# Kernel optimization log

Hardware: AMD Instinct MI355X
Metric: run time of the kernel (lower is better)

## Reference

```python
import jax, jax.numpy as jnp
import numpy as np

N_NODES = 100000
N_EDGES = 1600000
D_FEAT = 128
EPS = 0.0

def setup_inputs() -> dict:
    key = jax.random.key(0)
    k1, k2, k3 = jax.random.split(key, 3)
    feat = jax.random.normal(k1, (N_NODES, D_FEAT), dtype=jnp.float32)
    src = jax.random.randint(k2, (N_EDGES,), 0, N_NODES, dtype=jnp.int32)
    dst = jax.random.randint(k3, (N_EDGES,), 0, N_NODES, dtype=jnp.int32)
    return {"feat": feat, "src": src, "dst": dst}

def reference(feat, src, dst):
    # copy_u: gather messages from edge sources; sum-reduce into destinations
    msgs = feat[src]                                   # [E, D]
    neigh = jax.ops.segment_sum(msgs, dst, num_segments=N_NODES)  # [N, D]
    # (1 + eps) * feat_dst + aggregated neighbors
    return (1.0 + EPS) * feat + neigh
```

## Files before the change

kernel.cpp:

```cpp
#include <hip/hip_runtime.h>

#define D_FEAT 128
#define CAP 64
typedef unsigned int uint32;


__global__ void k_zero(uint32* __restrict__ p, int n) {
    int stride = gridDim.x * blockDim.x;
    for (int i = blockIdx.x * blockDim.x + threadIdx.x; i < n; i += stride)
        p[i] = 0u;
}

__global__ void k_fill_slack4(const int* __restrict__ src, const int* __restrict__ dst,
                              uint32* __restrict__ cur, int* __restrict__ adj, int e) {
    int i = blockIdx.x * blockDim.x + threadIdx.x;
    int nvec = e >> 2;
    if (i < nvec) {
        int4 s4 = ((const int4*)src)[i];
        int4 d4 = ((const int4*)dst)[i];
        uint32 p0 = atomicAdd(&cur[d4.x], 1u);
        uint32 p1 = atomicAdd(&cur[d4.y], 1u);
        uint32 p2 = atomicAdd(&cur[d4.z], 1u);
        uint32 p3 = atomicAdd(&cur[d4.w], 1u);
        if (p0 < CAP) adj[(size_t)d4.x * CAP + p0] = s4.x;
        if (p1 < CAP) adj[(size_t)d4.y * CAP + p1] = s4.y;
        if (p2 < CAP) adj[(size_t)d4.z * CAP + p2] = s4.z;
        if (p3 < CAP) adj[(size_t)d4.w * CAP + p3] = s4.w;
    }
    if (i == 0) {
        for (int k = nvec << 2; k < e; ++k) {
            int d = dst[k];
            uint32 p = atomicAdd(&cur[d], 1u);
            if (p < CAP) adj[(size_t)d * CAP + p] = src[k];
        }
    }
}

__global__ void k_gather4(const float4* __restrict__ feat4,
                          const uint32* __restrict__ deg,
                          const int* __restrict__ adj,
                          float4* __restrict__ out4, int n_nodes) {
    int gtid = blockIdx.x * blockDim.x + threadIdx.x;
    int wave = gtid >> 6;
    int lane = gtid & 63;
    int half = lane >> 5;
    int l    = lane & 31;
    int node = wave * 2 + half;
    if (node >= n_nodes) return;
    float4 acc = feat4[(size_t)node * 32 + l];
    int cnt = min((int)deg[node], CAP);
    for (int b = 0; b < cnt; b += 32) {
        int m = min(32, cnt - b);
        int a = (l < m) ? adj[(size_t)node * CAP + b + l] : 0;
        for (int j = 0; j < m; ++j) {
            int s = __shfl(a, j, 32);
            float4 v = feat4[(size_t)s * 32 + l];
            acc.x += v.x; acc.y += v.y; acc.z += v.z; acc.w += v.w;
        }
    }
    out4[(size_t)node * 32 + l] = acc;
}


__global__ void k_hist(const int* __restrict__ dst, uint32* __restrict__ deg, int e) {
    int i = blockIdx.x * blockDim.x + threadIdx.x;
    if (i < e) atomicAdd(&deg[dst[i]], 1u);
}

__global__ void k_scan1(const uint32* __restrict__ deg, uint32* __restrict__ offs,
                        uint32* __restrict__ bsum, int n) {
    __shared__ uint32 lds[256];
    int t = threadIdx.x;
    int i0 = blockIdx.x * 1024 + t * 4;
    uint32 v[4];
    for (int k = 0; k < 4; ++k) { int i = i0 + k; v[k] = (i < n) ? deg[i] : 0u; }
    uint32 tsum = v[0] + v[1] + v[2] + v[3];
    lds[t] = tsum; __syncthreads();
    uint32 run = tsum;
    for (int off = 1; off < 256; off <<= 1) {
        uint32 add = (t >= off) ? lds[t - off] : 0u; __syncthreads();
        run += add; lds[t] = run; __syncthreads();
    }
    uint32 p = run - tsum;
    for (int k = 0; k < 4; ++k) { int i = i0 + k; if (i < n) offs[i] = p; p += v[k]; }
    if (t == 255) bsum[blockIdx.x] = run;
}

__global__ void k_scan2(uint32* __restrict__ bsum, int nb) {
    __shared__ uint32 lds[256];
    int t = threadIdx.x;
    uint32 v = (t < nb) ? bsum[t] : 0u;
    lds[t] = v; __syncthreads();
    uint32 run = v;
    for (int off = 1; off < 256; off <<= 1) {
        uint32 add = (t >= off) ? lds[t - off] : 0u; __syncthreads();
        run += add; lds[t] = run; __syncthreads();
    }
    if (t < nb) bsum[t] = run - v;
}

__global__ void k_scan3(uint32* __restrict__ offs, uint32* __restrict__ cur,
                        const uint32* __restrict__ bsum, int n) {
    int i0 = blockIdx.x * 1024 + threadIdx.x * 4;
    uint32 add = bsum[blockIdx.x];
    for (int k = 0; k < 4; ++k) {
        int i = i0 + k;
        if (i < n) { uint32 o = offs[i] + add; offs[i] = o; cur[i] = o; }
    }
}

__global__ void k_fill(const int* __restrict__ src, const int* __restrict__ dst,
                       uint32* __restrict__ cur, int* __restrict__ adj, int e) {
    int i = blockIdx.x * blockDim.x + threadIdx.x;
    if (i < e) {
        int d = dst[i];
        uint32 p = atomicAdd(&cur[d], 1u);
        adj[p] = src[i];
    }
}

__global__ void k_gather(const float2* __restrict__ feat2,
                         const uint32* __restrict__ offs,
                         const uint32* __restrict__ endp,
                         const int* __restrict__ adj,
                         float2* __restrict__ out2, int n_nodes) {
    int gtid = blockIdx.x * blockDim.x + threadIdx.x;
    int node = gtid >> 6;
    int lane = gtid & 63;
    if (node >= n_nodes) return;
    float2 acc = feat2[(size_t)node * 64 + lane];
    int e0 = (int)offs[node];
    int e1 = (int)endp[node];
    for (int b = e0; b < e1; b += 64) {
        int cnt = min(64, e1 - b);
        int a = (lane < cnt) ? adj[b + lane] : 0;
        for (int j = 0; j < cnt; ++j) {
            int s = __shfl(a, j);
            float2 v = feat2[(size_t)s * 64 + lane];
            acc.x += v.x; acc.y += v.y;
        }
    }
    out2[(size_t)node * 64 + lane] = acc;
}


__global__ void init_out_kernel(const float4* __restrict__ feat,
                                float4* __restrict__ out, int n4) {
    int stride = gridDim.x * blockDim.x;
    for (int i = blockIdx.x * blockDim.x + threadIdx.x; i < n4; i += stride)
        out[i] = feat[i];
}

__global__ void scatter_edges_kernel(const float* __restrict__ feat,
                                     const int* __restrict__ src,
                                     const int* __restrict__ dst,
                                     float* __restrict__ out, int n_edges) {
    long long stride = (long long)gridDim.x * blockDim.x;
    long long total  = (long long)n_edges * 32;
    for (long long gtid = (long long)blockIdx.x * blockDim.x + threadIdx.x;
         gtid < total; gtid += stride) {
        int edge = (int)(gtid >> 5);
        int lane = (int)(gtid & 31);
        int s = src[edge];
        int d = dst[edge];
        const float4 v =
            *reinterpret_cast<const float4*>(feat + (size_t)s * D_FEAT + lane * 4);
        float* op = out + (size_t)d * D_FEAT + lane * 4;
        unsafeAtomicAdd(op + 0, v.x);
        unsafeAtomicAdd(op + 1, v.y);
        unsafeAtomicAdd(op + 2, v.z);
        unsafeAtomicAdd(op + 3, v.w);
    }
}

extern "C" void kernel_launch(void* const* d_in, const int* in_sizes, int n_in,
                              void* d_out, int out_size, void* d_ws, size_t ws_size,
                              hipStream_t stream) {
    const float* feat = (const float*)d_in[0];
    const int*   src  = (const int*)d_in[1];
    const int*   dst  = (const int*)d_in[2];
    float*       out  = (float*)d_out;

    int n_feat  = in_sizes[0];
    int n_edges = in_sizes[1];
    int n_nodes = n_feat / D_FEAT;
    int blk = 256;

    size_t need0 = ((size_t)n_nodes * CAP + n_nodes) * sizeof(uint32);
    if (ws_size >= need0) {
        int*    adj = (int*)d_ws;
        uint32* cur = (uint32*)(adj + (size_t)n_nodes * CAP);

        k_zero<<<256, blk, 0, stream>>>(cur, n_nodes);
        int nvec = n_edges >> 2;
        k_fill_slack4<<<(nvec + blk - 1) / blk, blk, 0, stream>>>(
            src, dst, cur, adj, n_edges);

        int nwaves = (n_nodes + 1) / 2;
        long long gthreads = (long long)nwaves * 64;
        k_gather4<<<(int)((gthreads + blk - 1) / blk), blk, 0, stream>>>(
            (const float4*)feat, cur, adj, (float4*)out, n_nodes);
        return;
    }

    int nb = (n_nodes + 1023) / 1024;
    size_t need1 = ((size_t)3 * n_nodes + 256 + (size_t)n_edges) * sizeof(uint32);
    if (ws_size >= need1 && nb <= 256) {
        uint32* deg  = (uint32*)d_ws;
        uint32* offs = deg  + n_nodes;
        uint32* cur  = offs + n_nodes;
        uint32* bsum = cur  + n_nodes;
        int*    adj  = (int*)(bsum + 256);

        k_zero <<<256, blk, 0, stream>>>(deg, n_nodes);
        k_hist <<<(n_edges + blk - 1) / blk, blk, 0, stream>>>(dst, deg, n_edges);
        k_scan1<<<nb, blk, 0, stream>>>(deg, offs, bsum, n_nodes);
        k_scan2<<<1, blk, 0, stream>>>(bsum, nb);
        k_scan3<<<nb, blk, 0, stream>>>(offs, cur, bsum, n_nodes);
        k_fill <<<(n_edges + blk - 1) / blk, blk, 0, stream>>>(src, dst, cur, adj, n_edges);

        long long gthreads = (long long)n_nodes * 64;
        k_gather<<<(int)((gthreads + blk - 1) / blk), blk, 0, stream>>>(
            (const float2*)feat, offs, cur, adj, (float2*)out, n_nodes);
        return;
    }

    int n4 = n_feat / 4;
    init_out_kernel<<<min((n4 + blk - 1) / blk, 2048), blk, 0, stream>>>(
        (const float4*)feat, (float4*)out, n4);
    long long total_threads = (long long)n_edges * 32;
    int grid_sc = (int)min((total_threads + blk - 1) / blk, (long long)8192);
    scatter_edges_kernel<<<grid_sc, blk, 0, stream>>>(feat, src, dst, out, n_edges);
}
```

Baseline: 349.7 us.

## Partition adjacency fill by destination range per XCD to localize atomics

Replaces the vectorized slack-fill kernel with one where each block is assigned a destination-node range keyed on blockIdx modulo 8, assuming round-robin block placement across the MI355X's XCDs. Each block scans a chunk of edges and only handles those whose destination falls in its range. The goal is to keep the atomic counters and adjacency writes for a node range inside one XCD's L2 and avoid cross-die coherence traffic. In exchange every edge's dst is read 8 times, and the int4 vectorized loads are dropped.

```diff
diff --git a/kernel.cpp b/kernel.cpp
--- a/kernel.cpp
+++ b/kernel.cpp
@@ -2,6 +2,8 @@
 
 #define D_FEAT 128
 #define CAP 64
+#define NXCD 8
+#define NCHUNK 768
 typedef unsigned int uint32;
 
 
@@ -11,27 +13,20 @@
         p[i] = 0u;
 }
 
-__global__ void k_fill_slack4(const int* __restrict__ src, const int* __restrict__ dst,
-                              uint32* __restrict__ cur, int* __restrict__ adj, int e) {
-    int i = blockIdx.x * blockDim.x + threadIdx.x;
-    int nvec = e >> 2;
-    if (i < nvec) {
-        int4 s4 = ((const int4*)src)[i];
-        int4 d4 = ((const int4*)dst)[i];
-        uint32 p0 = atomicAdd(&cur[d4.x], 1u);
-        uint32 p1 = atomicAdd(&cur[d4.y], 1u);
-        uint32 p2 = atomicAdd(&cur[d4.z], 1u);
-        uint32 p3 = atomicAdd(&cur[d4.w], 1u);
-        if (p0 < CAP) adj[(size_t)d4.x * CAP + p0] = s4.x;
-        if (p1 < CAP) adj[(size_t)d4.y * CAP + p1] = s4.y;
-        if (p2 < CAP) adj[(size_t)d4.z * CAP + p2] = s4.z;
-        if (p3 < CAP) adj[(size_t)d4.w * CAP + p3] = s4.w;
-    }
-    if (i == 0) {
-        for (int k = nvec << 2; k < e; ++k) {
-            int d = dst[k];
+__global__ void k_fill_xcd(const int* __restrict__ src, const int* __restrict__ dst,
+                           uint32* __restrict__ cur, int* __restrict__ adj,
+                           int e, int per, int rsize, int n_nodes) {
+    int xcd   = blockIdx.x & (NXCD - 1);
+    int chunk = blockIdx.x >> 3;
+    int lo = xcd * rsize;
+    int hi = min(lo + rsize, n_nodes);
+    int e0 = chunk * per;
+    int e1 = min(e0 + per, e);
+    for (int i = e0 + threadIdx.x; i < e1; i += blockDim.x) {
+        int d = dst[i];
+        if (d >= lo && d < hi) {
             uint32 p = atomicAdd(&cur[d], 1u);
-            if (p < CAP) adj[(size_t)d * CAP + p] = src[k];
+            if (p < CAP) adj[(size_t)d * CAP + p] = src[i];
         }
     }
 }
@@ -61,6 +56,16 @@
     out4[(size_t)node * 32 + l] = acc;
 }
 
+__global__ void k_fill_slack(const int* __restrict__ src, const int* __restrict__ dst,
+                             uint32* __restrict__ cur, int* __restrict__ adj, int e) {
+    int i = blockIdx.x * blockDim.x + threadIdx.x;
+    if (i < e) {
+        int d = dst[i];
+        uint32 p = atomicAdd(&cur[d], 1u);
+        if (p < CAP) adj[(size_t)d * CAP + p] = src[i];
+    }
+}
+
 
 __global__ void k_hist(const int* __restrict__ dst, uint32* __restrict__ deg, int e) {
     int i = blockIdx.x * blockDim.x + threadIdx.x;
@@ -192,9 +197,11 @@
         uint32* cur = (uint32*)(adj + (size_t)n_nodes * CAP);
 
         k_zero<<<256, blk, 0, stream>>>(cur, n_nodes);
-        int nvec = n_edges >> 2;
-        k_fill_slack4<<<(nvec + blk - 1) / blk, blk, 0, stream>>>(
-            src, dst, cur, adj, n_edges);
+
+        int per   = (n_edges + NCHUNK - 1) / NCHUNK;
+        int rsize = (n_nodes + NXCD - 1) / NXCD;
+        k_fill_xcd<<<NXCD * NCHUNK, blk, 0, stream>>>(
+            src, dst, cur, adj, n_edges, per, rsize, n_nodes);
 
         int nwaves = (n_nodes + 1) / 2;
         long long gthreads = (long long)nwaves * 64;
```

Measured after the change: 283.3 us. -19.0%, faster.
